# Kernel tuning notes

Measured on AMD Instinct MI355X. Metric: run time of the kernel, lower is better.

The kernel has to match this reference:

```python
import jax, jax.numpy as jnp
import numpy as np

N = 10000      # nodes
E = 160000     # edges
C = 128        # channels (hidden_irreps multiplicity)
NE = 10        # num_elements
G = 16         # num graphs
NB = 8         # num_bessel
RMAX = 5.0
PCUT = 5.0     # num_polynomial_cutoff
AVG_NN = 16.0
SQ3 = 3.0 ** 0.5


def _mlp(x, w1, w2, w3, wo):
    h = jax.nn.silu(x @ w1)
    h = jax.nn.silu(h @ w2)
    h = jax.nn.silu(h @ w3)
    return h @ wo


def _forward(positions, node_attrs, charges, shifts,
             W_emb, W_up1, Wr1_1, Wr1_2, Wr1_3, Wr1_o, Wlin1_s, Wlin1_v,
             P1_s1, P1_ss, P1_vv, P1_v1, P1_sv, Lp1_s, Lp1_v, R1,
             Wsk, Wup2_s, Wup2_v, Wr2_1, Wr2_2, Wr2_3, Wr2_o, Wlin2_s, Wlin2_v,
             P2_v1, P2_sv, Lp2_v, Rmid, Rout,
             edge_index, batch, num_graphs):
    snd, rcv = edge_index[0], edge_index[1]
    # edge vectors / lengths
    vec = positions[rcv] - positions[snd] + shifts                  # [E,3]
    length = jnp.sqrt(jnp.sum(vec * vec, -1) + 1e-12)               # [E]
    Yv = SQ3 * vec / length[:, None]                                # l=1 SH, component norm
    # Bessel radial basis * polynomial cutoff
    n = jnp.arange(1, NB + 1, dtype=positions.dtype)
    bess = (2.0 / RMAX) ** 0.5 * jnp.sin(n * jnp.pi * length[:, None] / RMAX) / length[:, None]
    u = length / RMAX
    p = PCUT
    fcut = jnp.where(u < 1.0,
                     1 - ((p + 1) * (p + 2) / 2) * u ** p + p * (p + 2) * u ** (p + 1)
                     - (p * (p + 1) / 2) * u ** (p + 2), 0.0)
    edge_feats = bess * fcut[:, None]                               # [E,NB]

    h = node_attrs @ W_emb                                          # node embedding [N,C]
    seg = lambda m: jax.ops.segment_sum(m, rcv, num_segments=N) / AVG_NN
    we = lambda Pm: node_attrs @ Pm                                 # element-dep. weights

    # ---- interaction / product / readout layer 1 (node feats are scalars) ----
    hu = h @ W_up1
    w = _mlp(edge_feats, Wr1_1, Wr1_2, Wr1_3, Wr1_o)                # [E,2C] TP weights
    w_ss, w_sv = w[:, :C], w[:, C:]
    hs_e = hu[snd]                                                  # gather sender feats
    A_s = seg(w_ss * hs_e)                                          # 0e x 0e -> 0e
    A_v = seg((w_sv * hs_e)[:, :, None] * Yv[:, None, :])           # 0e x 1o -> 1o
    A_s = A_s @ Wlin1_s
    A_v = jnp.einsum('ncd,ce->ned', A_v, Wlin1_v)
    # symmetric contraction (correlation=2), element-dependent weights
    B_s = we(P1_s1) * A_s + we(P1_ss) * A_s * A_s + we(P1_vv) * jnp.sum(A_v * A_v, -1) / SQ3
    B_v = we(P1_v1)[:, :, None] * A_v + we(P1_sv)[:, :, None] * A_s[:, :, None] * A_v
    h_s = B_s @ Lp1_s
    h_v = jnp.einsum('ncd,ce->ned', B_v, Lp1_v)
    dip1 = jnp.einsum('ncd,c->nd', h_v, R1)                         # linear dipole readout

    # ---- layer 2 (residual, output 128x1o) ----
    hs = h_s @ Wup2_s
    hv = jnp.einsum('ncd,ce->ned', h_v, Wup2_v)
    w2 = _mlp(edge_feats, Wr2_1, Wr2_2, Wr2_3, Wr2_o)               # [E,4C]
    w_a, w_b, w_c, w_d = w2[:, :C], w2[:, C:2 * C], w2[:, 2 * C:3 * C], w2[:, 3 * C:]
    hs_e, hv_e = hs[snd], hv[snd]
    m_s = w_a * hs_e + w_b * jnp.einsum('ecd,ed->ec', hv_e, Yv) / SQ3   # 0x0, 1x1->0
    m_v = (w_c * hs_e)[:, :, None] * Yv[:, None, :] + w_d[:, :, None] * hv_e  # 0x1,1x0->1
    A2_s = seg(m_s) @ Wlin2_s
    A2_v = jnp.einsum('ncd,ce->ned', seg(m_v), Wlin2_v)
    sc_v = jnp.einsum('ne,ecf,ncd->nfd', node_attrs, Wsk, h_v)      # skip TP (residual)
    B2_v = we(P2_v1)[:, :, None] * A2_v + we(P2_sv)[:, :, None] * A2_s[:, :, None] * A2_v
    h2_v = jnp.einsum('ncd,ce->ned', B2_v, Lp2_v) + sc_v
    # nonlinear dipole readout: input is pure 1o so gate scalars have no equivariant
    # path (zeros) -> sigmoid(0)=0.5 multiplier, as e3nn Gate would compute.
    mid = 0.5 * jnp.einsum('ncd,ck->nkd', h2_v, Rmid)               # [N,16,3]
    dip2 = jnp.einsum('nkd,k->nd', mid, Rout)

    atomic_dipoles = dip1 + dip2                                    # [N,3]
    total = jax.ops.segment_sum(atomic_dipoles, batch, num_segments=num_graphs)
    baseline = jax.ops.segment_sum(charges[:, None] * positions, batch, num_segments=num_graphs)
    return total + baseline, atomic_dipoles


def setup_inputs() -> dict:
    key = jax.random.key(0)
    ks = jax.random.split(key, 40)
    f32 = jnp.float32
    species = jax.random.randint(ks[0], (N,), 0, NE)
    w = lambda k, shape: jax.random.normal(k, shape, f32) / np.sqrt(shape[-2] if len(shape) > 1 else shape[0]).astype(np.float32)
    inp = dict(
        positions=jax.random.uniform(ks[1], (N, 3), f32) * 6.0,
        node_attrs=jax.nn.one_hot(species, NE, dtype=f32),
        charges=jax.random.normal(ks[2], (N,), f32),
        shifts=jnp.zeros((E, 3), f32),
        edge_index=jax.random.randint(ks[3], (2, E), 0, N),
        batch=jnp.sort(jax.random.randint(ks[4], (N,), 0, G)),
        ptr=jnp.arange(G + 1),
        W_emb=w(ks[5], (NE, C)), W_up1=w(ks[6], (C, C)),
        Wr1_1=w(ks[7], (NB, 64)), Wr1_2=w(ks[8], (64, 64)), Wr1_3=w(ks[9], (64, 64)),
        Wr1_o=w(ks[10], (64, 2 * C)), Wlin1_s=w(ks[11], (C, C)), Wlin1_v=w(ks[12], (C, C)),
        P1_s1=w(ks[13], (NE, C)), P1_ss=w(ks[14], (NE, C)), P1_vv=w(ks[15], (NE, C)),
        P1_v1=w(ks[16], (NE, C)), P1_sv=w(ks[17], (NE, C)),
        Lp1_s=w(ks[18], (C, C)), Lp1_v=w(ks[19], (C, C)),
        R1=jax.random.normal(ks[20], (C,), f32) / np.float32(np.sqrt(C)),
        Wsk=jax.random.normal(ks[21], (NE, C, C), f32) / np.float32(np.sqrt(C)),
        Wup2_s=w(ks[22], (C, C)), Wup2_v=w(ks[23], (C, C)),
        Wr2_1=w(ks[24], (NB, 64)), Wr2_2=w(ks[25], (64, 64)), Wr2_3=w(ks[26], (64, 64)),
        Wr2_o=w(ks[27], (64, 4 * C)), Wlin2_s=w(ks[28], (C, C)), Wlin2_v=w(ks[29], (C, C)),
        P2_v1=w(ks[30], (NE, C)), P2_sv=w(ks[31], (NE, C)), Lp2_v=w(ks[32], (C, C)),
        Rmid=w(ks[33], (C, 16)),
        Rout=jax.random.normal(ks[34], (16,), f32) / 4.0,
    )
    return inp


def reference(positions, node_attrs, charges, shifts, edge_index, batch, ptr,
              W_emb, W_up1, Wr1_1, Wr1_2, Wr1_3, Wr1_o, Wlin1_s, Wlin1_v,
              P1_s1, P1_ss, P1_vv, P1_v1, P1_sv, Lp1_s, Lp1_v, R1,
              Wsk, Wup2_s, Wup2_v, Wr2_1, Wr2_2, Wr2_3, Wr2_o, Wlin2_s, Wlin2_v,
              P2_v1, P2_sv, Lp2_v, Rmid, Rout):
    num_graphs = ptr.shape[0] - 1
    return _forward(positions, node_attrs, charges, shifts,
                    W_emb, W_up1, Wr1_1, Wr1_2, Wr1_3, Wr1_o, Wlin1_s, Wlin1_v,
                    P1_s1, P1_ss, P1_vv, P1_v1, P1_sv, Lp1_s, Lp1_v, R1,
                    Wsk, Wup2_s, Wup2_v, Wr2_1, Wr2_2, Wr2_3, Wr2_o, Wlin2_s, Wlin2_v,
                    P2_v1, P2_sv, Lp2_v, Rmid, Rout,
                    edge_index, batch, num_graphs)
```

## Files before the change

### kernel.cpp

```cpp
#include <hip/hip_runtime.h>

#define NN 10000
#define EE 160000
#define CC 128
#define NEL 10
#define NGR 16

static inline int cdiv(int a, int b) { return (a + b - 1) / b; }

__device__ __forceinline__ float silu_f(float x) { return x / (1.0f + __expf(-x)); }

__device__ __forceinline__ float bf2f(unsigned short u) {
    unsigned int x = ((unsigned int)u) << 16;
    return __uint_as_float(x);
}
__device__ __forceinline__ unsigned short f2bf(float f) {
    unsigned int x = __float_as_uint(f);
    unsigned int r = x + 0x7fffu + ((x >> 16) & 1u);
    return (unsigned short)(r >> 16);
}

typedef __attribute__((ext_vector_type(8))) short bf16x8;
typedef __attribute__((ext_vector_type(4))) float f32x4;

template <int K, int N, int MODE>
__global__ __launch_bounds__(256) void mfma_gemm(
    const unsigned short* __restrict__ in, int in_ld,
    const unsigned short* __restrict__ Wt,
    unsigned short* __restrict__ out, int out_ld,
    int R)
{
    constexpr int NT = N / 16;
    constexpr int KC = K / 32;
    constexpr int CPR = K / 8;
    __shared__ __align__(16) unsigned short Ash[64 * K];
    __shared__ __align__(16) unsigned short Bsh[N * K];

    const int tid = threadIdx.x;
    const int w = tid >> 6;
    const int l = tid & 63;
    const int row0 = blockIdx.x * 64;
    const int cb = blockIdx.y * N;

    for (int cid = tid; cid < 64 * CPR; cid += 256) {
        int r = cid / CPR, k8 = cid % CPR;
        int row = row0 + r;
        uint4 val = make_uint4(0u, 0u, 0u, 0u);
        if (row < R) val = *(const uint4*)(in + (size_t)row * in_ld + k8 * 8);
        unsigned bo = ((unsigned)(r * K + k8 * 8) * 2u) ^ (((unsigned)(r & 7)) << 4);
        *(uint4*)((char*)Ash + bo) = val;
    }
    for (int cid = tid; cid < N * CPR; cid += 256) {
        int nn = cid / CPR, k8 = cid % CPR;
        uint4 val = *(const uint4*)(Wt + (size_t)(cb + nn) * K + k8 * 8);
        unsigned bo = ((unsigned)(nn * K + k8 * 8) * 2u) ^ (((unsigned)(nn & 7)) << 4);
        *(uint4*)((char*)Bsh + bo) = val;
    }
    __syncthreads();

    bf16x8 afr[KC];
#pragma unroll
    for (int kc = 0; kc < KC; ++kc) {
        int r = w * 16 + (l & 15);
        int k = kc * 32 + (l >> 4) * 8;
        unsigned bo = ((unsigned)(r * K + k) * 2u) ^ (((unsigned)(r & 7)) << 4);
        afr[kc] = *(const bf16x8*)((char*)Ash + bo);
    }

    f32x4 acc[NT];
#pragma unroll
    for (int nt = 0; nt < NT; ++nt) {
        acc[nt] = (f32x4){0.f, 0.f, 0.f, 0.f};
#pragma unroll
        for (int kc = 0; kc < KC; ++kc) {
            int col = nt * 16 + (l & 15);
            int k = kc * 32 + (l >> 4) * 8;
            unsigned bo = ((unsigned)(col * K + k) * 2u) ^ (((unsigned)(col & 7)) << 4);
            bf16x8 bfr = *(const bf16x8*)((char*)Bsh + bo);
            acc[nt] = __builtin_amdgcn_mfma_f32_16x16x32_bf16(afr[kc], bfr, acc[nt], 0, 0, 0);
        }
    }

#pragma unroll
    for (int nt = 0; nt < NT; ++nt) {
#pragma unroll
        for (int rg = 0; rg < 4; ++rg) {
            int row = row0 + w * 16 + (l >> 4) * 4 + rg;
            if (row < R) {
                int col = cb + nt * 16 + (l & 15);
                float v = acc[nt][rg];
                if constexpr (MODE == 1) v = silu_f(v);
                out[(size_t)row * out_ld + col] = f2bf(v);
            }
        }
    }
}

template <int K, int N, int MODE>
__global__ __launch_bounds__(256) void mfma_gemm_f32(
    const float* __restrict__ in, int in_ld,
    const unsigned short* __restrict__ Wt,
    float* __restrict__ out, int out_ld,
    int R, float scale)
{
    constexpr int NT = N / 16;
    constexpr int KC = K / 32;
    constexpr int CPR = K / 8;
    __shared__ __align__(16) unsigned short Ash[64 * K];
    __shared__ __align__(16) unsigned short Bsh[N * K];

    const int tid = threadIdx.x;
    const int w = tid >> 6;
    const int l = tid & 63;
    const int row0 = blockIdx.x * 64;
    const int cb = blockIdx.y * N;

    for (int cid = tid; cid < 64 * CPR; cid += 256) {
        int r = cid / CPR, k8 = cid % CPR;
        int row = row0 + r;
        union { unsigned short u16[8]; uint4 v; } pk;
        if (row < R) {
            const float* p = in + (size_t)row * in_ld + k8 * 8;
            float4 f0 = *(const float4*)p;
            float4 f1 = *(const float4*)(p + 4);
            pk.u16[0] = f2bf(f0.x); pk.u16[1] = f2bf(f0.y);
            pk.u16[2] = f2bf(f0.z); pk.u16[3] = f2bf(f0.w);
            pk.u16[4] = f2bf(f1.x); pk.u16[5] = f2bf(f1.y);
            pk.u16[6] = f2bf(f1.z); pk.u16[7] = f2bf(f1.w);
        } else {
            pk.v = make_uint4(0u, 0u, 0u, 0u);
        }
        unsigned bo = ((unsigned)(r * K + k8 * 8) * 2u) ^ (((unsigned)(r & 7)) << 4);
        *(uint4*)((char*)Ash + bo) = pk.v;
    }
    for (int cid = tid; cid < N * CPR; cid += 256) {
        int nn = cid / CPR, k8 = cid % CPR;
        uint4 val = *(const uint4*)(Wt + (size_t)(cb + nn) * K + k8 * 8);
        unsigned bo = ((unsigned)(nn * K + k8 * 8) * 2u) ^ (((unsigned)(nn & 7)) << 4);
        *(uint4*)((char*)Bsh + bo) = val;
    }
    __syncthreads();

    bf16x8 afr[KC];
#pragma unroll
    for (int kc = 0; kc < KC; ++kc) {
        int r = w * 16 + (l & 15);
        int k = kc * 32 + (l >> 4) * 8;
        unsigned bo = ((unsigned)(r * K + k) * 2u) ^ (((unsigned)(r & 7)) << 4);
        afr[kc] = *(const bf16x8*)((char*)Ash + bo);
    }

    f32x4 acc[NT];
#pragma unroll
    for (int nt = 0; nt < NT; ++nt) {
        acc[nt] = (f32x4){0.f, 0.f, 0.f, 0.f};
#pragma unroll
        for (int kc = 0; kc < KC; ++kc) {
            int col = nt * 16 + (l & 15);
            int k = kc * 32 + (l >> 4) * 8;
            unsigned bo = ((unsigned)(col * K + k) * 2u) ^ (((unsigned)(col & 7)) << 4);
            bf16x8 bfr = *(const bf16x8*)((char*)Bsh + bo);
            acc[nt] = __builtin_amdgcn_mfma_f32_16x16x32_bf16(afr[kc], bfr, acc[nt], 0, 0, 0);
        }
    }

#pragma unroll
    for (int nt = 0; nt < NT; ++nt) {
#pragma unroll
        for (int rg = 0; rg < 4; ++rg) {
            int row = row0 + w * 16 + (l >> 4) * 4 + rg;
            if (row < R) {
                int col = cb + nt * 16 + (l & 15);
                float v = acc[nt][rg] * scale;
                size_t idx = (size_t)row * out_ld + col;
                if constexpr (MODE == 6) out[idx] += v;
                else out[idx] = v;
            }
        }
    }
}

__global__ void k_wprep(const float* __restrict__ src, unsigned short* __restrict__ dst,
                        int K, int N, int Kpad)
{
    int i = blockIdx.x * 256 + threadIdx.x;
    if (i >= N * Kpad) return;
    int n = i / Kpad, k = i % Kpad;
    dst[i] = (k < K) ? f2bf(src[k * N + n]) : (unsigned short)0;
}

struct WP10 { const float* s[10]; unsigned short* d[10]; };
__global__ void k_wprep10(WP10 wp)
{
    int m = blockIdx.y;
    int i = blockIdx.x * 256 + threadIdx.x;
    if (i >= 128 * 128) return;
    int n = i / 128, k = i % 128;
    wp.d[m][i] = f2bf(wp.s[m][k * 128 + n]);
}

__global__ void k_count(const int* __restrict__ rcv, int* __restrict__ deg)
{
    int e = blockIdx.x * 256 + threadIdx.x;
    if (e < EE) atomicAdd(&deg[rcv[e]], 1);
}

__global__ __launch_bounds__(256) void k_scan(const int* __restrict__ deg,
                                              int* __restrict__ rowptr,
                                              int* __restrict__ cursor)
{
    __shared__ int part[256];
    const int t = threadIdx.x;
    const int PER = (NN + 255) / 256;
    int base = t * PER;
    int s = 0;
    for (int j = 0; j < PER; ++j) { int idx = base + j; if (idx < NN) s += deg[idx]; }
    part[t] = s;
    __syncthreads();
    for (int off = 1; off < 256; off <<= 1) {
        int v = (t >= off) ? part[t - off] : 0;
        __syncthreads();
        part[t] += v;
        __syncthreads();
    }
    int run = (t == 0) ? 0 : part[t - 1];
    for (int j = 0; j < PER; ++j) {
        int idx = base + j;
        if (idx < NN) { rowptr[idx] = run; cursor[idx] = run; run += deg[idx]; }
    }
    if (t == 255) rowptr[NN] = part[255];
}

__global__ void k_fill(const int* __restrict__ rcv, int* __restrict__ cursor,
                       int* __restrict__ perm)
{
    int e = blockIdx.x * 256 + threadIdx.x;
    if (e >= EE) return;
    int pos = atomicAdd(&cursor[rcv[e]], 1);
    perm[pos] = e;
}

__global__ __launch_bounds__(256) void k_sortwave(const int* __restrict__ rowptr,
                                                  int* __restrict__ perm)
{
    int gid = blockIdx.x * 256 + threadIdx.x;
    int wid = gid >> 6;
    int lane = gid & 63;
    if (wid >= NN) return;
    int a = rowptr[wid], b = rowptr[wid + 1];
    int d = b - a;
    if (d <= 1) return;
    if (d <= 64) {
        int v = (lane < d) ? perm[a + lane] : 0x7fffffff;
        int rank = 0;
        for (int j = 0; j < 64; ++j) {
            int vj = __shfl(v, j);
            if (j < d && vj < v) ++rank;
        }
        if (lane < d) perm[a + rank] = v;
    } else if (lane == 0) {
        for (int i = a + 1; i < b; ++i) {
            int v = perm[i]; int j = i - 1;
            while (j >= a && perm[j] > v) { perm[j + 1] = perm[j]; --j; }
            perm[j + 1] = v;
        }
    }
}

__global__ void k_geom_perm(const float* __restrict__ pos, const float* __restrict__ shifts,
                            const int* __restrict__ snd, const int* __restrict__ rcv,
                            const int* __restrict__ perm,
                            float* __restrict__ Yv, unsigned short* __restrict__ efb,
                            int* __restrict__ psnd)
{
    int i = blockIdx.x * 256 + threadIdx.x;
    if (i >= EE) return;
    int e = perm[i];
    int s = snd[e], r = rcv[e];
    psnd[i] = s;
    float vx = pos[r * 3 + 0] - pos[s * 3 + 0] + shifts[e * 3 + 0];
    float vy = pos[r * 3 + 1] - pos[s * 3 + 1] + shifts[e * 3 + 1];
    float vz = pos[r * 3 + 2] - pos[s * 3 + 2] + shifts[e * 3 + 2];
    float len = sqrtf(vx * vx + vy * vy + vz * vz + 1e-12f);
    float inv = 1.0f / len;
    const float SQ3 = 1.7320508075688772f;
    Yv[i * 3 + 0] = SQ3 * vx * inv;
    Yv[i * 3 + 1] = SQ3 * vy * inv;
    Yv[i * 3 + 2] = SQ3 * vz * inv;
    float u = len * 0.2f;
    float fc = 0.0f;
    if (u < 1.0f) {
        float u2 = u * u, u4 = u2 * u2, u5 = u4 * u, u6 = u5 * u, u7 = u6 * u;
        fc = 1.0f - 21.0f * u5 + 35.0f * u6 - 15.0f * u7;
    }
    float pref = 0.6324555320336759f * inv * fc;
    const float PIO5 = 0.6283185307179586f;
    union { unsigned short u16[8]; uint4 v; } pk;
#pragma unroll
    for (int n = 1; n <= 8; ++n)
        pk.u16[n - 1] = f2bf(pref * sinf((float)n * PIO5 * len));
    uint4* dst = (uint4*)(efb + (size_t)i * 32);
    dst[0] = pk.v;
    dst[1] = make_uint4(0u, 0u, 0u, 0u);
    dst[2] = make_uint4(0u, 0u, 0u, 0u);
    dst[3] = make_uint4(0u, 0u, 0u, 0u);
}

__global__ __launch_bounds__(256) void k_gather1(
    const int* __restrict__ rowptr, const int* __restrict__ psnd,
    const float* __restrict__ Yv, const unsigned short* __restrict__ wb,
    int e0, int e1,
    const float* __restrict__ gS,
    float* __restrict__ outS, float* __restrict__ outV)
{
    const int t = threadIdx.x;
    const int c = t & 127;
    const int n = blockIdx.x * 2 + (t >> 7);
    if (n >= NN) return;
    int rs = rowptr[n], re = rowptr[n + 1];
    if (rs < e0) rs = e0;
    if (re > e1) re = e1;
    if (rs >= re) return;
    float accs = 0.f, a0 = 0.f, a1 = 0.f, a2 = 0.f;
    for (int i = rs; i < re; ++i) {
        const unsigned short* wp = wb + (size_t)(i - e0) * 256;
        float wss = bf2f(wp[c]);
        float wsv = bf2f(wp[128 + c]);
        float h = gS[psnd[i] * 128 + c];
        float y0 = Yv[i * 3], y1 = Yv[i * 3 + 1], y2 = Yv[i * 3 + 2];
        accs = fmaf(wss, h, accs);
        float tv = wsv * h;
        a0 = fmaf(tv, y0, a0); a1 = fmaf(tv, y1, a1); a2 = fmaf(tv, y2, a2);
    }
    outS[n * 128 + c] += accs;
    outV[n * 384 + c]       += a0;
    outV[n * 384 + 128 + c] += a1;
    outV[n * 384 + 256 + c] += a2;
}

__global__ __launch_bounds__(256) void k_gather23(
    const int* __restrict__ rowptr, const int* __restrict__ psnd,
    const float* __restrict__ Yv, const unsigned short* __restrict__ wb,
    int e0, int e1,
    const float* __restrict__ gS, const float* __restrict__ gV,
    float* __restrict__ outS, float* __restrict__ outV)
{
    const int t = threadIdx.x;
    const int c = t & 127;
    const int n = blockIdx.x * 2 + (t >> 7);
    if (n >= NN) return;
    int rs = rowptr[n], re = rowptr[n + 1];
    if (rs < e0) rs = e0;
    if (re > e1) re = e1;
    if (rs >= re) return;
    float accs = 0.f, a0 = 0.f, a1 = 0.f, a2 = 0.f;
    for (int i = rs; i < re; ++i) {
        const unsigned short* wp = wb + (size_t)(i - e0) * 512;
        float wa = bf2f(wp[c]);
        float wbv = bf2f(wp[128 + c]);
        float wc = bf2f(wp[256 + c]);
        float wd = bf2f(wp[384 + c]);
        int s = psnd[i];
        float hs = gS[s * 128 + c];
        float v0 = gV[s * 384 + c];
        float v1 = gV[s * 384 + 128 + c];
        float v2 = gV[s * 384 + 256 + c];
        float y0 = Yv[i * 3], y1 = Yv[i * 3 + 1], y2 = Yv[i * 3 + 2];
        float hd = v0 * y0 + v1 * y1 + v2 * y2;
        accs = fmaf(wa, hs, accs);
        accs = fmaf(wbv, hd * 0.57735026919f, accs);
        float tv = wc * hs;
        a0 = fmaf(tv, y0, a0); a0 = fmaf(wd, v0, a0);
        a1 = fmaf(tv, y1, a1); a1 = fmaf(wd, v1, a1);
        a2 = fmaf(tv, y2, a2); a2 = fmaf(wd, v2, a2);
    }
    outS[n * 128 + c] += accs;
    outV[n * 384 + c]       += a0;
    outV[n * 384 + 128 + c] += a1;
    outV[n * 384 + 256 + c] += a2;
}

__global__ void k_species(const float* __restrict__ attrs, int* __restrict__ species)
{
    int n = blockIdx.x * 256 + threadIdx.x;
    if (n >= NN) return;
    int sp = 0;
#pragma unroll
    for (int j = 0; j < NEL; ++j)
        if (attrs[n * NEL + j] > 0.5f) sp = j;
    species[n] = sp;
}

__global__ void k_embed(const float* __restrict__ W_emb, const int* __restrict__ species,
                        float* __restrict__ h)
{
    int t = blockIdx.x * 256 + threadIdx.x;
    if (t >= NN * CC) return;
    int n = t >> 7, c = t & 127;
    h[t] = W_emb[species[n] * CC + c];
}

__global__ void k_rmix(const float* __restrict__ Rmid, const float* __restrict__ Rout,
                       float* __restrict__ rmix)
{
    int c = threadIdx.x;
    float s = 0.f;
#pragma unroll
    for (int k = 0; k < 16; ++k) s = fmaf(Rmid[c * 16 + k], Rout[k], s);
    rmix[c] = s;
}

__global__ void k_B1(const int* __restrict__ species,
                     const float* __restrict__ As_l, const float* __restrict__ Av_l,
                     const float* __restrict__ P_s1, const float* __restrict__ P_ss,
                     const float* __restrict__ P_vv, const float* __restrict__ P_v1,
                     const float* __restrict__ P_sv,
                     float* __restrict__ Bs, float* __restrict__ Bv)
{
    int t = blockIdx.x * 256 + threadIdx.x;
    if (t >= NN * CC) return;
    int n = t >> 7, c = t & 127;
    int sp = species[n];
    int pb = sp * CC + c;
    int vb = n * 384 + c;
    float as = As_l[t];
    float a0 = Av_l[vb], a1 = Av_l[vb + CC], a2 = Av_l[vb + 2 * CC];
    Bs[t] = P_s1[pb] * as + P_ss[pb] * as * as
          + P_vv[pb] * (a0 * a0 + a1 * a1 + a2 * a2) * 0.57735026919f;
    float tv = P_v1[pb] + P_sv[pb] * as;
    Bv[vb] = tv * a0; Bv[vb + CC] = tv * a1; Bv[vb + 2 * CC] = tv * a2;
}

__global__ void k_B2(const int* __restrict__ species,
                     const float* __restrict__ As_l, const float* __restrict__ Av_l,
                     const float* __restrict__ P_v1, const float* __restrict__ P_sv,
                     float* __restrict__ Bv)
{
    int t = blockIdx.x * 256 + threadIdx.x;
    if (t >= NN * CC) return;
    int n = t >> 7, c = t & 127;
    int sp = species[n];
    int pb = sp * CC + c;
    int vb = n * 384 + c;
    float as = As_l[t];
    float tv = P_v1[pb] + P_sv[pb] * as;
    Bv[vb] = tv * Av_l[vb];
    Bv[vb + CC] = tv * Av_l[vb + CC];
    Bv[vb + 2 * CC] = tv * Av_l[vb + 2 * CC];
}

__global__ void k_dip1(const float* __restrict__ h_v, const float* __restrict__ R1,
                       float* __restrict__ dip1)
{
    int n = blockIdx.x, l = threadIdx.x;
    const float* hb = h_v + n * 384;
#pragma unroll
    for (int d = 0; d < 3; ++d) {
        float v = hb[d * CC + l] * R1[l] + hb[d * CC + 64 + l] * R1[64 + l];
        for (int o = 32; o > 0; o >>= 1) v += __shfl_down(v, o);
        if (l == 0) dip1[n * 3 + d] = v;
    }
}

__global__ void k_sc(const int* __restrict__ species, const float* __restrict__ h_v,
                     const float* __restrict__ Wsk, float* __restrict__ h2v)
{
    int n = blockIdx.x, f = threadIdx.x;
    int sp = species[n];
    const float* Wp = Wsk + sp * (CC * CC);
    const float* hvn = h_v + n * 384;
    float a0 = 0.f, a1 = 0.f, a2 = 0.f;
    for (int c = 0; c < CC; ++c) {
        float w = Wp[c * CC + f];
        a0 = fmaf(hvn[c], w, a0);
        a1 = fmaf(hvn[CC + c], w, a1);
        a2 = fmaf(hvn[2 * CC + c], w, a2);
    }
    h2v[n * 384 + f] = a0;
    h2v[n * 384 + CC + f] = a1;
    h2v[n * 384 + 2 * CC + f] = a2;
}

__global__ void k_node_out(const float* __restrict__ h2v, const float* __restrict__ rmix,
                           const float* __restrict__ dip1,
                           const float* __restrict__ charges, const float* __restrict__ pos,
                           float* __restrict__ out, float* __restrict__ tot)
{
    int n = blockIdx.x, l = threadIdx.x;
    const float* hb = h2v + n * 384;
    float r0 = rmix[l], r1 = rmix[64 + l];
    float red[3];
#pragma unroll
    for (int d = 0; d < 3; ++d) {
        float v = hb[d * CC + l] * r0 + hb[d * CC + 64 + l] * r1;
        for (int o = 32; o > 0; o >>= 1) v += __shfl_down(v, o);
        red[d] = v;
    }
    if (l == 0) {
        float q = charges[n];
#pragma unroll
        for (int d = 0; d < 3; ++d) {
            float a = dip1[n * 3 + d] + 0.5f * red[d];
            out[48 + n * 3 + d] = a;
            tot[n * 3 + d] = a + q * pos[n * 3 + d];
        }
    }
}

__global__ __launch_bounds__(256) void k_greduce(const float* __restrict__ tot,
                                                 const int* __restrict__ batch,
                                                 float* __restrict__ out)
{
    __shared__ float r[256 * 3];
    const int g = blockIdx.x;
    const int t = threadIdx.x;
    float s0 = 0.f, s1 = 0.f, s2 = 0.f;
    for (int n = t; n < NN; n += 256) {
        if (batch[n] == g) {
            s0 += tot[n * 3]; s1 += tot[n * 3 + 1]; s2 += tot[n * 3 + 2];
        }
    }
    r[t] = s0; r[256 + t] = s1; r[512 + t] = s2;
    __syncthreads();
    for (int off = 128; off > 0; off >>= 1) {
        if (t < off) {
            r[t] += r[t + off];
            r[256 + t] += r[256 + t + off];
            r[512 + t] += r[512 + t + off];
        }
        __syncthreads();
    }
    if (t < 3) out[g * 3 + t] = r[t * 256];
}

extern "C" void kernel_launch(void* const* d_in, const int* in_sizes, int n_in,
                              void* d_out, int out_size, void* d_ws, size_t ws_size,
                              hipStream_t stream)
{
    const float* positions = (const float*)d_in[0];
    const float* node_attrs = (const float*)d_in[1];
    const float* charges = (const float*)d_in[2];
    const float* shifts = (const float*)d_in[3];
    const int*   eidx = (const int*)d_in[4];
    const int*   batch = (const int*)d_in[5];
    const float* W_emb  = (const float*)d_in[7];
    const float* W_up1  = (const float*)d_in[8];
    const float* Wr1_1  = (const float*)d_in[9];
    const float* Wr1_2  = (const float*)d_in[10];
    const float* Wr1_3  = (const float*)d_in[11];
    const float* Wr1_o  = (const float*)d_in[12];
    const float* Wlin1_s = (const float*)d_in[13];
    const float* Wlin1_v = (const float*)d_in[14];
    const float* P1_s1 = (const float*)d_in[15];
    const float* P1_ss = (const float*)d_in[16];
    const float* P1_vv = (const float*)d_in[17];
    const float* P1_v1 = (const float*)d_in[18];
    const float* P1_sv = (const float*)d_in[19];
    const float* Lp1_s = (const float*)d_in[20];
    const float* Lp1_v = (const float*)d_in[21];
    const float* R1    = (const float*)d_in[22];
    const float* Wsk   = (const float*)d_in[23];
    const float* Wup2_s = (const float*)d_in[24];
    const float* Wup2_v = (const float*)d_in[25];
    const float* Wr2_1 = (const float*)d_in[26];
    const float* Wr2_2 = (const float*)d_in[27];
    const float* Wr2_3 = (const float*)d_in[28];
    const float* Wr2_o = (const float*)d_in[29];
    const float* Wlin2_s = (const float*)d_in[30];
    const float* Wlin2_v = (const float*)d_in[31];
    const float* P2_v1 = (const float*)d_in[32];
    const float* P2_sv = (const float*)d_in[33];
    const float* Lp2_v = (const float*)d_in[34];
    const float* Rmid  = (const float*)d_in[35];
    const float* Rout  = (const float*)d_in[36];
    (void)in_sizes; (void)n_in; (void)out_size;

    const int* snd = eidx;
    const int* rcv = eidx + EE;
    float* out = (float*)d_out;

    char* ws = (char*)d_ws;
    size_t off = 0;
    auto alloc = [&](size_t bytes) -> void* {
        void* p = (void*)(ws + off);
        off = (off + bytes + 255) & ~(size_t)255;
        return p;
    };
    int*   species = (int*)alloc((size_t)NN * 4);
    int*   deg     = (int*)alloc((size_t)NN * 4);
    int*   rowptr  = (int*)alloc((size_t)(NN + 16) * 4);
    int*   cursor  = (int*)alloc((size_t)NN * 4);
    int*   perm    = (int*)alloc((size_t)EE * 4);
    int*   psnd    = (int*)alloc((size_t)EE * 4);
    float* Yv   = (float*)alloc((size_t)EE * 3 * 4);
    unsigned short* efb = (unsigned short*)alloc((size_t)EE * 32 * 2);
    float* A_s  = (float*)alloc((size_t)NN * CC * 4);
    float* A_v  = (float*)alloc((size_t)NN * 3 * CC * 4);
    float* hbuf = (float*)alloc((size_t)NN * CC * 4);
    float* hu   = (float*)alloc((size_t)NN * CC * 4);
    float* h_v  = (float*)alloc((size_t)NN * 3 * CC * 4);
    float* hv   = (float*)alloc((size_t)NN * 3 * CC * 4);
    float* h2v  = (float*)alloc((size_t)NN * 3 * CC * 4);
    float* dip1 = (float*)alloc((size_t)NN * 3 * 4);
    float* rmix = (float*)alloc((size_t)CC * 4);
    float* tot  = (float*)alloc((size_t)NN * 3 * 4);
    unsigned short* W1t_l1 = (unsigned short*)alloc(64 * 32 * 2);
    unsigned short* W2t_l1 = (unsigned short*)alloc(64 * 64 * 2);
    unsigned short* W3t_l1 = (unsigned short*)alloc(64 * 64 * 2);
    unsigned short* Wot_l1 = (unsigned short*)alloc(256 * 64 * 2);
    unsigned short* W1t_l2 = (unsigned short*)alloc(64 * 32 * 2);
    unsigned short* W2t_l2 = (unsigned short*)alloc(64 * 64 * 2);
    unsigned short* W3t_l2 = (unsigned short*)alloc(64 * 64 * 2);
    unsigned short* Wot_l2 = (unsigned short*)alloc(512 * 64 * 2);
    unsigned short* Wn[10];
    for (int m = 0; m < 10; ++m) Wn[m] = (unsigned short*)alloc(128 * 128 * 2);
    unsigned short* hbA = (unsigned short*)alloc((size_t)EE * 64 * 2);
    unsigned short* hbB = (unsigned short*)alloc((size_t)EE * 64 * 2);

    int C = 16;
    if (off + (size_t)(EE / 4) * 512 * 2 + 4096 <= ws_size) C = 4;
    else if (off + (size_t)(EE / 8) * 512 * 2 + 4096 <= ws_size) C = 8;
    const int EC = EE / C;
    unsigned short* wbuf = (unsigned short*)alloc((size_t)EC * 512 * 2);

    const float inv16 = 1.0f / 16.0f;
    const float one = 1.0f;

    hipMemsetAsync(deg, 0, (size_t)NN * 4, stream);
    hipMemsetAsync(A_s, 0, (size_t)NN * CC * 4, stream);
    hipMemsetAsync(A_v, 0, (size_t)NN * 3 * CC * 4, stream);

    k_wprep<<<cdiv(64 * 32, 256), 256, 0, stream>>>(Wr1_1, W1t_l1, 8, 64, 32);
    k_wprep<<<cdiv(64 * 64, 256), 256, 0, stream>>>(Wr1_2, W2t_l1, 64, 64, 64);
    k_wprep<<<cdiv(64 * 64, 256), 256, 0, stream>>>(Wr1_3, W3t_l1, 64, 64, 64);
    k_wprep<<<cdiv(256 * 64, 256), 256, 0, stream>>>(Wr1_o, Wot_l1, 64, 256, 64);
    k_wprep<<<cdiv(64 * 32, 256), 256, 0, stream>>>(Wr2_1, W1t_l2, 8, 64, 32);
    k_wprep<<<cdiv(64 * 64, 256), 256, 0, stream>>>(Wr2_2, W2t_l2, 64, 64, 64);
    k_wprep<<<cdiv(64 * 64, 256), 256, 0, stream>>>(Wr2_3, W3t_l2, 64, 64, 64);
    k_wprep<<<cdiv(512 * 64, 256), 256, 0, stream>>>(Wr2_o, Wot_l2, 64, 512, 64);
    {
        WP10 wp;
        const float* srcs[10] = {W_up1, Wlin1_s, Wlin1_v, Lp1_s, Lp1_v,
                                 Wup2_s, Wup2_v, Wlin2_s, Wlin2_v, Lp2_v};
        for (int m = 0; m < 10; ++m) { wp.s[m] = srcs[m]; wp.d[m] = Wn[m]; }
        k_wprep10<<<dim3(cdiv(128 * 128, 256), 10), 256, 0, stream>>>(wp);
    }

    k_count<<<cdiv(EE, 256), 256, 0, stream>>>(rcv, deg);
    k_scan<<<1, 256, 0, stream>>>(deg, rowptr, cursor);
    k_fill<<<cdiv(EE, 256), 256, 0, stream>>>(rcv, cursor, perm);
    k_sortwave<<<cdiv(NN * 64, 256), 256, 0, stream>>>(rowptr, perm);
    k_geom_perm<<<cdiv(EE, 256), 256, 0, stream>>>(positions, shifts, snd, rcv, perm, Yv, efb, psnd);

    k_species<<<cdiv(NN, 256), 256, 0, stream>>>(node_attrs, species);
    k_embed<<<cdiv(NN * CC, 256), 256, 0, stream>>>(W_emb, species, hbuf);
    k_rmix<<<1, CC, 0, stream>>>(Rmid, Rout, rmix);

    mfma_gemm_f32<128, 128, 0><<<cdiv(NN, 64), 256, 0, stream>>>(
        hbuf, 128, Wn[0], hu, 128, NN, one);

    mfma_gemm<32, 64, 1><<<cdiv(EE, 64), 256, 0, stream>>>(efb, 32, W1t_l1, hbA, 64, EE);
    mfma_gemm<64, 64, 1><<<cdiv(EE, 64), 256, 0, stream>>>(hbA, 64, W2t_l1, hbB, 64, EE);
    mfma_gemm<64, 64, 1><<<cdiv(EE, 64), 256, 0, stream>>>(hbB, 64, W3t_l1, hbA, 64, EE);
    for (int ch = 0; ch < C; ++ch) {
        int e0 = ch * EC, e1 = e0 + EC;
        mfma_gemm<64, 128, 2><<<dim3(cdiv(EC, 64), 2), 256, 0, stream>>>(
            hbA + (size_t)e0 * 64, 64, Wot_l1, wbuf, 256, EC);
        k_gather1<<<NN / 2, 256, 0, stream>>>(
            rowptr, psnd, Yv, wbuf, e0, e1, hu, A_s, A_v);
    }

    mfma_gemm_f32<128, 128, 0><<<cdiv(NN, 64), 256, 0, stream>>>(
        A_s, 128, Wn[1], A_s, 128, NN, inv16);
    mfma_gemm_f32<128, 128, 0><<<cdiv(3 * NN, 64), 256, 0, stream>>>(
        A_v, 128, Wn[2], A_v, 128, 3 * NN, inv16);
    k_B1<<<cdiv(NN * CC, 256), 256, 0, stream>>>(
        species, A_s, A_v, P1_s1, P1_ss, P1_vv, P1_v1, P1_sv, hbuf , A_v );
    mfma_gemm_f32<128, 128, 0><<<cdiv(NN, 64), 256, 0, stream>>>(
        hbuf, 128, Wn[3], hu , 128, NN, one);
    mfma_gemm_f32<128, 128, 0><<<cdiv(3 * NN, 64), 256, 0, stream>>>(
        A_v , 128, Wn[4], h_v, 128, 3 * NN, one);
    k_dip1<<<NN, 64, 0, stream>>>(h_v, R1, dip1);
    mfma_gemm_f32<128, 128, 0><<<cdiv(NN, 64), 256, 0, stream>>>(
        hu , 128, Wn[5], hbuf , 128, NN, one);
    mfma_gemm_f32<128, 128, 0><<<cdiv(3 * NN, 64), 256, 0, stream>>>(
        h_v, 128, Wn[6], hv, 128, 3 * NN, one);

    hipMemsetAsync(A_s, 0, (size_t)NN * CC * 4, stream);
    hipMemsetAsync(A_v, 0, (size_t)NN * 3 * CC * 4, stream);
    mfma_gemm<32, 64, 1><<<cdiv(EE, 64), 256, 0, stream>>>(efb, 32, W1t_l2, hbA, 64, EE);
    mfma_gemm<64, 64, 1><<<cdiv(EE, 64), 256, 0, stream>>>(hbA, 64, W2t_l2, hbB, 64, EE);
    mfma_gemm<64, 64, 1><<<cdiv(EE, 64), 256, 0, stream>>>(hbB, 64, W3t_l2, hbA, 64, EE);
    for (int ch = 0; ch < C; ++ch) {
        int e0 = ch * EC, e1 = e0 + EC;
        mfma_gemm<64, 128, 2><<<dim3(cdiv(EC, 64), 4), 256, 0, stream>>>(
            hbA + (size_t)e0 * 64, 64, Wot_l2, wbuf, 512, EC);
        k_gather23<<<NN / 2, 256, 0, stream>>>(
            rowptr, psnd, Yv, wbuf, e0, e1, hbuf , hv, A_s, A_v);
    }

    mfma_gemm_f32<128, 128, 0><<<cdiv(NN, 64), 256, 0, stream>>>(
        A_s, 128, Wn[7], A_s, 128, NN, inv16);
    mfma_gemm_f32<128, 128, 0><<<cdiv(3 * NN, 64), 256, 0, stream>>>(
        A_v, 128, Wn[8], A_v, 128, 3 * NN, inv16);
    k_sc<<<NN, 128, 0, stream>>>(species, h_v, Wsk, h2v);
    k_B2<<<cdiv(NN * CC, 256), 256, 0, stream>>>(species, A_s, A_v, P2_v1, P2_sv, A_v );
    mfma_gemm_f32<128, 128, 6><<<cdiv(3 * NN, 64), 256, 0, stream>>>(
        A_v , 128, Wn[9], h2v, 128, 3 * NN, one);

    k_node_out<<<NN, 64, 0, stream>>>(h2v, rmix, dip1, charges, positions, out, tot);
    k_greduce<<<NGR, 256, 0, stream>>>(tot, batch, out);
}
```

Before: 614.6 us.

## Store gathered node features in bf16 and allow fewer edge chunks

```diff
diff --git a/kernel.cpp b/kernel.cpp
--- a/kernel.cpp
+++ b/kernel.cpp
@@ -173,20 +173,23 @@
                 int col = cb + nt * 16 + (l & 15);
                 float v = acc[nt][rg] * scale;
                 size_t idx = (size_t)row * out_ld + col;
-                if constexpr (MODE == 6) out[idx] += v;
-                else out[idx] = v;
+                if constexpr (MODE == 6)      out[idx] += v;
+                else if constexpr (MODE == 2) ((unsigned short*)out)[idx] = f2bf(v);
+                else                          out[idx] = v;
             }
         }
     }
 }
 
-__global__ void k_wprep(const float* __restrict__ src, unsigned short* __restrict__ dst,
-                        int K, int N, int Kpad)
-{
+struct WPE { const float* s[8]; unsigned short* d[8]; int K[8], N[8], Kp[8]; };
+__global__ void k_wprepE(WPE wp)
+{
+    int m = blockIdx.y;
     int i = blockIdx.x * 256 + threadIdx.x;
-    if (i >= N * Kpad) return;
-    int n = i / Kpad, k = i % Kpad;
-    dst[i] = (k < K) ? f2bf(src[k * N + n]) : (unsigned short)0;
+    int tot = wp.N[m] * wp.Kp[m];
+    if (i >= tot) return;
+    int n = i / wp.Kp[m], k = i % wp.Kp[m];
+    wp.d[m][i] = (k < wp.K[m]) ? f2bf(wp.s[m][k * wp.N[m] + n]) : (unsigned short)0;
 }
 
 struct WP10 { const float* s[10]; unsigned short* d[10]; };
@@ -310,7 +313,7 @@
     const int* __restrict__ rowptr, const int* __restrict__ psnd,
     const float* __restrict__ Yv, const unsigned short* __restrict__ wb,
     int e0, int e1,
-    const float* __restrict__ gS,
+    const unsigned short* __restrict__ gS,
     float* __restrict__ outS, float* __restrict__ outV)
 {
     const int t = threadIdx.x;
@@ -326,7 +329,7 @@
         const unsigned short* wp = wb + (size_t)(i - e0) * 256;
         float wss = bf2f(wp[c]);
         float wsv = bf2f(wp[128 + c]);
-        float h = gS[psnd[i] * 128 + c];
+        float h = bf2f(gS[psnd[i] * 128 + c]);
         float y0 = Yv[i * 3], y1 = Yv[i * 3 + 1], y2 = Yv[i * 3 + 2];
         accs = fmaf(wss, h, accs);
         float tv = wsv * h;
@@ -342,7 +345,7 @@
     const int* __restrict__ rowptr, const int* __restrict__ psnd,
     const float* __restrict__ Yv, const unsigned short* __restrict__ wb,
     int e0, int e1,
-    const float* __restrict__ gS, const float* __restrict__ gV,
+    const unsigned short* __restrict__ gS, const unsigned short* __restrict__ gV,
     float* __restrict__ outS, float* __restrict__ outV)
 {
     const int t = threadIdx.x;
@@ -361,10 +364,10 @@
         float wc = bf2f(wp[256 + c]);
         float wd = bf2f(wp[384 + c]);
         int s = psnd[i];
-        float hs = gS[s * 128 + c];
-        float v0 = gV[s * 384 + c];
-        float v1 = gV[s * 384 + 128 + c];
-        float v2 = gV[s * 384 + 256 + c];
+        float hs = bf2f(gS[s * 128 + c]);
+        float v0 = bf2f(gV[s * 384 + c]);
+        float v1 = bf2f(gV[s * 384 + 128 + c]);
+        float v2 = bf2f(gV[s * 384 + 256 + c]);
         float y0 = Yv[i * 3], y1 = Yv[i * 3 + 1], y2 = Yv[i * 3 + 2];
         float hd = v0 * y0 + v1 * y1 + v2 * y2;
         accs = fmaf(wa, hs, accs);
@@ -599,11 +602,13 @@
     float* hbuf = (float*)alloc((size_t)NN * CC * 4);
     float* hu   = (float*)alloc((size_t)NN * CC * 4);
     float* h_v  = (float*)alloc((size_t)NN * 3 * CC * 4);
-    float* hv   = (float*)alloc((size_t)NN * 3 * CC * 4);
     float* h2v  = (float*)alloc((size_t)NN * 3 * CC * 4);
     float* dip1 = (float*)alloc((size_t)NN * 3 * 4);
     float* rmix = (float*)alloc((size_t)CC * 4);
     float* tot  = (float*)alloc((size_t)NN * 3 * 4);
+    unsigned short* hub = (unsigned short*)alloc((size_t)NN * CC * 2);
+    unsigned short* hsb = (unsigned short*)alloc((size_t)NN * CC * 2);
+    unsigned short* hvb = (unsigned short*)alloc((size_t)NN * 3 * CC * 2);
     unsigned short* W1t_l1 = (unsigned short*)alloc(64 * 32 * 2);
     unsigned short* W2t_l1 = (unsigned short*)alloc(64 * 64 * 2);
     unsigned short* W3t_l1 = (unsigned short*)alloc(64 * 64 * 2);
@@ -618,8 +623,10 @@
     unsigned short* hbB = (unsigned short*)alloc((size_t)EE * 64 * 2);
 
     int C = 16;
-    if (off + (size_t)(EE / 4) * 512 * 2 + 4096 <= ws_size) C = 4;
-    else if (off + (size_t)(EE / 8) * 512 * 2 + 4096 <= ws_size) C = 8;
+    if      (off + (size_t)EE * 512 * 2 + 4096 <= ws_size)        C = 1;
+    else if (off + (size_t)(EE / 2) * 512 * 2 + 4096 <= ws_size)  C = 2;
+    else if (off + (size_t)(EE / 4) * 512 * 2 + 4096 <= ws_size)  C = 4;
+    else if (off + (size_t)(EE / 8) * 512 * 2 + 4096 <= ws_size)  C = 8;
     const int EC = EE / C;
     unsigned short* wbuf = (unsigned short*)alloc((size_t)EC * 512 * 2);
 
@@ -630,14 +637,16 @@
     hipMemsetAsync(A_s, 0, (size_t)NN * CC * 4, stream);
     hipMemsetAsync(A_v, 0, (size_t)NN * 3 * CC * 4, stream);
 
-    k_wprep<<<cdiv(64 * 32, 256), 256, 0, stream>>>(Wr1_1, W1t_l1, 8, 64, 32);
-    k_wprep<<<cdiv(64 * 64, 256), 256, 0, stream>>>(Wr1_2, W2t_l1, 64, 64, 64);
-    k_wprep<<<cdiv(64 * 64, 256), 256, 0, stream>>>(Wr1_3, W3t_l1, 64, 64, 64);
-    k_wprep<<<cdiv(256 * 64, 256), 256, 0, stream>>>(Wr1_o, Wot_l1, 64, 256, 64);
-    k_wprep<<<cdiv(64 * 32, 256), 256, 0, stream>>>(Wr2_1, W1t_l2, 8, 64, 32);
-    k_wprep<<<cdiv(64 * 64, 256), 256, 0, stream>>>(Wr2_2, W2t_l2, 64, 64, 64);
-    k_wprep<<<cdiv(64 * 64, 256), 256, 0, stream>>>(Wr2_3, W3t_l2, 64, 64, 64);
-    k_wprep<<<cdiv(512 * 64, 256), 256, 0, stream>>>(Wr2_o, Wot_l2, 64, 512, 64);
+    {
+        WPE wp;
+        const float* s[8] = {Wr1_1, Wr1_2, Wr1_3, Wr1_o, Wr2_1, Wr2_2, Wr2_3, Wr2_o};
+        unsigned short* d[8] = {W1t_l1, W2t_l1, W3t_l1, Wot_l1, W1t_l2, W2t_l2, W3t_l2, Wot_l2};
+        int Ks[8] = {8, 64, 64, 64, 8, 64, 64, 64};
+        int Ns[8] = {64, 64, 64, 256, 64, 64, 64, 512};
+        int Kp[8] = {32, 64, 64, 64, 32, 64, 64, 64};
+        for (int m = 0; m < 8; ++m) { wp.s[m] = s[m]; wp.d[m] = d[m]; wp.K[m] = Ks[m]; wp.N[m] = Ns[m]; wp.Kp[m] = Kp[m]; }
+        k_wprepE<<<dim3(cdiv(512 * 64, 256), 8), 256, 0, stream>>>(wp);
+    }
     {
         WP10 wp;
         const float* srcs[10] = {W_up1, Wlin1_s, Wlin1_v, Lp1_s, Lp1_v,
@@ -656,8 +665,8 @@
     k_embed<<<cdiv(NN * CC, 256), 256, 0, stream>>>(W_emb, species, hbuf);
     k_rmix<<<1, CC, 0, stream>>>(Rmid, Rout, rmix);
 
-    mfma_gemm_f32<128, 128, 0><<<cdiv(NN, 64), 256, 0, stream>>>(
-        hbuf, 128, Wn[0], hu, 128, NN, one);
+    mfma_gemm_f32<128, 128, 2><<<cdiv(NN, 64), 256, 0, stream>>>(
+        hbuf, 128, Wn[0], (float*)hub, 128, NN, one);
 
     mfma_gemm<32, 64, 1><<<cdiv(EE, 64), 256, 0, stream>>>(efb, 32, W1t_l1, hbA, 64, EE);
     mfma_gemm<64, 64, 1><<<cdiv(EE, 64), 256, 0, stream>>>(hbA, 64, W2t_l1, hbB, 64, EE);
@@ -667,7 +676,7 @@
         mfma_gemm<64, 128, 2><<<dim3(cdiv(EC, 64), 2), 256, 0, stream>>>(
             hbA + (size_t)e0 * 64, 64, Wot_l1, wbuf, 256, EC);
         k_gather1<<<NN / 2, 256, 0, stream>>>(
-            rowptr, psnd, Yv, wbuf, e0, e1, hu, A_s, A_v);
+            rowptr, psnd, Yv, wbuf, e0, e1, hub, A_s, A_v);
     }
 
     mfma_gemm_f32<128, 128, 0><<<cdiv(NN, 64), 256, 0, stream>>>(
@@ -681,10 +690,10 @@
     mfma_gemm_f32<128, 128, 0><<<cdiv(3 * NN, 64), 256, 0, stream>>>(
         A_v , 128, Wn[4], h_v, 128, 3 * NN, one);
     k_dip1<<<NN, 64, 0, stream>>>(h_v, R1, dip1);
-    mfma_gemm_f32<128, 128, 0><<<cdiv(NN, 64), 256, 0, stream>>>(
-        hu , 128, Wn[5], hbuf , 128, NN, one);
-    mfma_gemm_f32<128, 128, 0><<<cdiv(3 * NN, 64), 256, 0, stream>>>(
-        h_v, 128, Wn[6], hv, 128, 3 * NN, one);
+    mfma_gemm_f32<128, 128, 2><<<cdiv(NN, 64), 256, 0, stream>>>(
+        hu , 128, Wn[5], (float*)hsb, 128, NN, one);
+    mfma_gemm_f32<128, 128, 2><<<cdiv(3 * NN, 64), 256, 0, stream>>>(
+        h_v, 128, Wn[6], (float*)hvb, 128, 3 * NN, one);
 
     hipMemsetAsync(A_s, 0, (size_t)NN * CC * 4, stream);
     hipMemsetAsync(A_v, 0, (size_t)NN * 3 * CC * 4, stream);
@@ -696,7 +705,7 @@
         mfma_gemm<64, 128, 2><<<dim3(cdiv(EC, 64), 4), 256, 0, stream>>>(
             hbA + (size_t)e0 * 64, 64, Wot_l2, wbuf, 512, EC);
         k_gather23<<<NN / 2, 256, 0, stream>>>(
-            rowptr, psnd, Yv, wbuf, e0, e1, hbuf , hv, A_s, A_v);
+            rowptr, psnd, Yv, wbuf, e0, e1, hsb, hvb, A_s, A_v);
     }
 
     mfma_gemm_f32<128, 128, 0><<<cdiv(NN, 64), 256, 0, stream>>>(
```

Result: faster. 530.0 us (-13.8%).
